# Kernel optimization log

Measured on AMD Instinct MI355X. Metric: run time of the kernel, lower is better.

Reference implementation:

```python
import jax, jax.numpy as jnp
import numpy as np

N, E, F_IN, H, C, L = 50000, 800000, 128, 128, 47, 3
BN_EPS = 1e-5


def setup_inputs() -> dict:
    key = jax.random.key(0)
    ks = jax.random.split(key, 12)
    s = 0.1
    return {
        "x": jax.random.normal(ks[0], (N, F_IN), jnp.float32),
        "edge_index": jax.random.randint(ks[1], (2, E), 0, N, jnp.int32),
        # stacked GINConv MLP params (in_channels == hidden so all layers stack)
        "W1": jax.random.normal(ks[2], (L, F_IN, H), jnp.float32) * s,
        "b1": jnp.full((L, H), 0.01, jnp.float32),
        "gamma": jnp.ones((L, H), jnp.float32),
        "beta": jnp.zeros((L, H), jnp.float32),
        "bn_mean": jnp.zeros((L, H), jnp.float32),
        "bn_var": jnp.ones((L, H), jnp.float32),
        "W2": jax.random.normal(ks[3], (L, H, H), jnp.float32) * s,
        "b2": jnp.full((L, H), 0.01, jnp.float32),
        # head
        "lw1": jax.random.normal(ks[4], (H, H), jnp.float32) * s,
        "lb1": jnp.zeros((H,), jnp.float32),
        "lw2": jax.random.normal(ks[5], (H, C), jnp.float32) * s,
        "lb2": jnp.zeros((C,), jnp.float32),
    }


def reference(x, edge_index, W1, b1, gamma, beta, bn_mean, bn_var, W2, b2, lw1, lb1, lw2, lb2):
    src, dst = edge_index[0], edge_index[1]
    h = x
    for i in range(L):
        # GINConv: nn((1 + eps) * x + sum_{j in N(i)} x_j), eps = 0
        agg = jax.ops.segment_sum(h[src], dst, num_segments=N)  # [N, H] scatter-sum
        z = agg + h
        z = z @ W1[i] + b1[i]
        # BatchNorm1d in eval mode (running stats)
        z = (z - bn_mean[i]) * jax.lax.rsqrt(bn_var[i] + BN_EPS) * gamma[i] + beta[i]
        z = jax.nn.relu(z)
        h = jax.nn.relu(z @ W2[i] + b2[i])
    h = jax.nn.relu(h @ lw1 + lb1)
    # dropout disabled (eval mode)
    logits = h @ lw2 + lb2
    return jax.nn.log_softmax(logits, axis=-1)
```

## Files before the change

### kernel.cpp

```cpp
#include <hip/hip_runtime.h>
#include <math.h>

#define NN 50000
#define EE 800000
#define HH 128
#define LL 3
#define CC 47
#define CAP 64
#define FILL_B 2048
#define NT_TILES 782

typedef _Float16 half8 __attribute__((ext_vector_type(8)));
typedef float    f32x4 __attribute__((ext_vector_type(4)));
typedef unsigned short us8 __attribute__((ext_vector_type(8)));

__device__ __forceinline__ f32x4 mfma16(half8 a, half8 b, f32x4 c) {
    return __builtin_amdgcn_mfma_f32_16x16x32_f16(a, b, c, 0, 0, 0);
}

__global__ void k_fill_prep(const int* __restrict__ ei, int* __restrict__ cursor,
                            unsigned short* __restrict__ csr,
                            const float* __restrict__ x, const float* __restrict__ W1,
                            const float* __restrict__ W2, const float* __restrict__ lw1,
                            const float* __restrict__ lw2, const float* __restrict__ b1,
                            const float* __restrict__ gamma, const float* __restrict__ beta,
                            const float* __restrict__ bnm, const float* __restrict__ bnv,
                            _Float16* __restrict__ xh, _Float16* __restrict__ hb0,
                            _Float16* __restrict__ hb1, _Float16* __restrict__ Wt1h,
                            _Float16* __restrict__ Wt2h, _Float16* __restrict__ lw1t,
                            _Float16* __restrict__ lw2t, float* __restrict__ A1f,
                            float* __restrict__ B1f) {
    if (blockIdx.x < FILL_B) {
        const int part = blockIdx.x & 7;
        const int chunk = blockIdx.x >> 3;
        const int nchunks = FILL_B >> 3;
        const int lo = part * (NN / 8);
        const int hi = (part == 7) ? NN : lo + (NN / 8);
        for (int e = chunk * 256 + threadIdx.x; e < EE; e += nchunks * 256) {
            const int d = ei[EE + e];
            if (d >= lo && d < hi) {
                const int pos = atomicAdd(&cursor[d], 1);
                if (pos < CAP) csr[(d << 6) + pos] = (unsigned short)ei[e];
            }
        }
        return;
    }
    const int i = (blockIdx.x - FILL_B) * 256 + threadIdx.x;
    const int Q0 = (NN * HH) / 8;
    const int Q1 = Q0 + LL * HH * HH;
    const int Q2 = Q1 + LL * HH * HH;
    const int Q3 = Q2 + HH * HH;
    const int Q4 = Q3 + 48 * HH;
    const int Q5 = Q4 + LL * HH;
    const int Q6 = Q5 + 3 * HH;
    if (i < Q0) {
        const f32x4* xp = (const f32x4*)x + (size_t)i * 2;
        f32x4 u = xp[0], v = xp[1];
        half8 o;
        o[0] = (_Float16)u[0]; o[1] = (_Float16)u[1]; o[2] = (_Float16)u[2]; o[3] = (_Float16)u[3];
        o[4] = (_Float16)v[0]; o[5] = (_Float16)v[1]; o[6] = (_Float16)v[2]; o[7] = (_Float16)v[3];
        *((half8*)xh + i) = o;
    } else if (i < Q1) {
        int j = i - Q0;
        int l = j / (HH * HH);
        int n = (j / HH) % HH;
        int k = j % HH;
        Wt1h[l * HH * HH + n * HH + k] = (_Float16)W1[l * HH * HH + k * HH + n];
    } else if (i < Q2) {
        int j = i - Q1;
        int l = j / (HH * HH);
        int n = (j / HH) % HH;
        int k = j % HH;
        Wt2h[l * HH * HH + n * HH + k] = (_Float16)W2[l * HH * HH + k * HH + n];
    } else if (i < Q3) {
        int j = i - Q2;
        int n = j / HH, k = j % HH;
        lw1t[n * HH + k] = (_Float16)lw1[k * HH + n];
    } else if (i < Q4) {
        int j = i - Q3;
        int n = j / HH, k = j % HH;
        lw2t[n * HH + k] = (_Float16)((n < CC) ? lw2[k * CC + n] : 0.f);
    } else if (i < Q5) {
        int j = i - Q4;
        float s = gamma[j] * rsqrtf(bnv[j] + 1e-5f);
        A1f[j] = s;
        B1f[j] = (b1[j] - bnm[j]) * s + beta[j];
    } else if (i < Q6) {
        int j = i - Q5;
        int b = j >> 7, k = j & 127;
        _Float16* t = (b == 0) ? xh : ((b == 1) ? hb0 : hb1);
        t[(size_t)NN * HH + k] = (_Float16)0.f;
    }
}

__device__ __forceinline__ void gather_tile(
    const _Float16* __restrict__ hin, const int* __restrict__ degs,
    const unsigned short* __restrict__ csr, _Float16* Ab, int tile0, int tid, int fo) {
#pragma unroll
    for (int pass = 0; pass < 4; ++pass) {
        const int r = pass * 16 + (tid >> 4);
        const int g = tile0 + r;
        const int gg = (g < NN) ? g : NN;
        float a[8];
        half8 hv = *(const half8*)(hin + (size_t)gg * HH + fo);
#pragma unroll
        for (int j = 0; j < 8; ++j) a[j] = (float)hv[j];
        int d = (g < NN) ? degs[g] : 0;
        d = (d < CAP) ? d : CAP;
        const unsigned short* crow = csr + (gg << 6);
        for (int kk = 0; kk < d; kk += 8) {
            us8 sv = *(const us8*)(crow + kk);
            int s[8];
#pragma unroll
            for (int j = 0; j < 8; ++j) s[j] = (kk + j < d) ? (int)sv[j] : NN;
            half8 v[8];
#pragma unroll
            for (int j = 0; j < 8; ++j) v[j] = *(const half8*)(hin + (size_t)s[j] * HH + fo);
#pragma unroll
            for (int j = 0; j < 8; ++j) {
#pragma unroll
                for (int t = 0; t < 8; ++t) a[t] += (float)v[j][t];
            }
        }
        half8 o;
#pragma unroll
        for (int j = 0; j < 8; ++j) o[j] = (_Float16)a[j];
        *(half8*)(Ab + r * 136 + fo) = o;
    }
}

__global__ __launch_bounds__(256, 4) void k_layer(
    const _Float16* __restrict__ hin, _Float16* __restrict__ hout,
    const _Float16* __restrict__ Wt1, const _Float16* __restrict__ Wt2,
    const float* __restrict__ A1, const float* __restrict__ B1,
    const float* __restrict__ b2, const int* __restrict__ degs,
    const unsigned short* __restrict__ csr) {
    __shared__ _Float16 Ab[64 * 136];
    const int tid = threadIdx.x;
    const int wave = tid >> 6, lane = tid & 63;
    const int q = lane >> 4, l15 = lane & 15;
    const int tile0 = blockIdx.x * 64;
    const int fo = (tid & 15) * 8;

    half8 Bf[2][4];
#pragma unroll
    for (int t = 0; t < 2; ++t)
#pragma unroll
        for (int kt = 0; kt < 4; ++kt)
            Bf[t][kt] = *(const half8*)(Wt1 + (wave * 32 + t * 16 + l15) * 128 + kt * 32 + q * 8);

    gather_tile(hin, degs, csr, Ab, tile0, tid, fo);
    __syncthreads();

    f32x4 acc[4][2];
#pragma unroll
    for (int s = 0; s < 4; ++s)
#pragma unroll
        for (int t = 0; t < 2; ++t) acc[s][t] = (f32x4){0.f, 0.f, 0.f, 0.f};
#pragma unroll
    for (int kt = 0; kt < 4; ++kt) {
        const int ko = kt * 32 + q * 8;
        half8 a0 = *(const half8*)(Ab + (0 * 16 + l15) * 136 + ko);
        half8 a1 = *(const half8*)(Ab + (1 * 16 + l15) * 136 + ko);
        half8 a2 = *(const half8*)(Ab + (2 * 16 + l15) * 136 + ko);
        half8 a3 = *(const half8*)(Ab + (3 * 16 + l15) * 136 + ko);
        acc[0][0] = mfma16(a0, Bf[0][kt], acc[0][0]);
        acc[1][0] = mfma16(a1, Bf[0][kt], acc[1][0]);
        acc[2][0] = mfma16(a2, Bf[0][kt], acc[2][0]);
        acc[3][0] = mfma16(a3, Bf[0][kt], acc[3][0]);
        acc[0][1] = mfma16(a0, Bf[1][kt], acc[0][1]);
        acc[1][1] = mfma16(a1, Bf[1][kt], acc[1][1]);
        acc[2][1] = mfma16(a2, Bf[1][kt], acc[2][1]);
        acc[3][1] = mfma16(a3, Bf[1][kt], acc[3][1]);
    }
#pragma unroll
    for (int t = 0; t < 2; ++t)
#pragma unroll
        for (int kt = 0; kt < 4; ++kt)
            Bf[t][kt] = *(const half8*)(Wt2 + (wave * 32 + t * 16 + l15) * 128 + kt * 32 + q * 8);
    __syncthreads();

#pragma unroll
    for (int t = 0; t < 2; ++t) {
        const int col = wave * 32 + t * 16 + l15;
        const float sc = A1[col], sh = B1[col];
#pragma unroll
        for (int s = 0; s < 4; ++s)
#pragma unroll
            for (int r = 0; r < 4; ++r) {
                const int row = s * 16 + q * 4 + r;
                float v = acc[s][t][r] * sc + sh;
                Ab[row * 136 + col] = (_Float16)fmaxf(v, 0.f);
            }
    }
    __syncthreads();

#pragma unroll
    for (int s = 0; s < 4; ++s)
#pragma unroll
        for (int t = 0; t < 2; ++t) acc[s][t] = (f32x4){0.f, 0.f, 0.f, 0.f};
#pragma unroll
    for (int kt = 0; kt < 4; ++kt) {
        const int ko = kt * 32 + q * 8;
        half8 a0 = *(const half8*)(Ab + (0 * 16 + l15) * 136 + ko);
        half8 a1 = *(const half8*)(Ab + (1 * 16 + l15) * 136 + ko);
        half8 a2 = *(const half8*)(Ab + (2 * 16 + l15) * 136 + ko);
        half8 a3 = *(const half8*)(Ab + (3 * 16 + l15) * 136 + ko);
        acc[0][0] = mfma16(a0, Bf[0][kt], acc[0][0]);
        acc[1][0] = mfma16(a1, Bf[0][kt], acc[1][0]);
        acc[2][0] = mfma16(a2, Bf[0][kt], acc[2][0]);
        acc[3][0] = mfma16(a3, Bf[0][kt], acc[3][0]);
        acc[0][1] = mfma16(a0, Bf[1][kt], acc[0][1]);
        acc[1][1] = mfma16(a1, Bf[1][kt], acc[1][1]);
        acc[2][1] = mfma16(a2, Bf[1][kt], acc[2][1]);
        acc[3][1] = mfma16(a3, Bf[1][kt], acc[3][1]);
    }
#pragma unroll
    for (int t = 0; t < 2; ++t) {
        const int col = wave * 32 + t * 16 + l15;
        const float bb = b2[col];
#pragma unroll
        for (int s = 0; s < 4; ++s)
#pragma unroll
            for (int r = 0; r < 4; ++r) {
                const int row = s * 16 + q * 4 + r;
                const int g = tile0 + row;
                if (g < NN) {
                    float v = fmaxf(acc[s][t][r] + bb, 0.f);
                    hout[(size_t)g * HH + col] = (_Float16)v;
                }
            }
    }
}

__global__ __launch_bounds__(256, 4) void k_layer_head(
    const _Float16* __restrict__ hin,
    const _Float16* __restrict__ Wt1, const _Float16* __restrict__ Wt2,
    const float* __restrict__ A1, const float* __restrict__ B1,
    const float* __restrict__ b2,
    const _Float16* __restrict__ lw1t, const _Float16* __restrict__ lw2t,
    const float* __restrict__ lb1, const float* __restrict__ lb2,
    float* __restrict__ out, const int* __restrict__ degs,
    const unsigned short* __restrict__ csr) {
    __shared__ _Float16 Ab[64 * 136];
    const int tid = threadIdx.x;
    const int wave = tid >> 6, lane = tid & 63;
    const int q = lane >> 4, l15 = lane & 15;
    const int tile0 = blockIdx.x * 64;
    const int fo = (tid & 15) * 8;

    half8 Bf[2][4];
#pragma unroll
    for (int t = 0; t < 2; ++t)
#pragma unroll
        for (int kt = 0; kt < 4; ++kt)
            Bf[t][kt] = *(const half8*)(Wt1 + (wave * 32 + t * 16 + l15) * 128 + kt * 32 + q * 8);

    gather_tile(hin, degs, csr, Ab, tile0, tid, fo);
    __syncthreads();

    f32x4 acc[4][2];
#pragma unroll
    for (int s = 0; s < 4; ++s)
#pragma unroll
        for (int t = 0; t < 2; ++t) acc[s][t] = (f32x4){0.f, 0.f, 0.f, 0.f};
#pragma unroll
    for (int kt = 0; kt < 4; ++kt) {
        const int ko = kt * 32 + q * 8;
        half8 a0 = *(const half8*)(Ab + (0 * 16 + l15) * 136 + ko);
        half8 a1 = *(const half8*)(Ab + (1 * 16 + l15) * 136 + ko);
        half8 a2 = *(const half8*)(Ab + (2 * 16 + l15) * 136 + ko);
        half8 a3 = *(const half8*)(Ab + (3 * 16 + l15) * 136 + ko);
        acc[0][0] = mfma16(a0, Bf[0][kt], acc[0][0]);
        acc[1][0] = mfma16(a1, Bf[0][kt], acc[1][0]);
        acc[2][0] = mfma16(a2, Bf[0][kt], acc[2][0]);
        acc[3][0] = mfma16(a3, Bf[0][kt], acc[3][0]);
        acc[0][1] = mfma16(a0, Bf[1][kt], acc[0][1]);
        acc[1][1] = mfma16(a1, Bf[1][kt], acc[1][1]);
        acc[2][1] = mfma16(a2, Bf[1][kt], acc[2][1]);
        acc[3][1] = mfma16(a3, Bf[1][kt], acc[3][1]);
    }
#pragma unroll
    for (int t = 0; t < 2; ++t)
#pragma unroll
        for (int kt = 0; kt < 4; ++kt)
            Bf[t][kt] = *(const half8*)(Wt2 + (wave * 32 + t * 16 + l15) * 128 + kt * 32 + q * 8);
    __syncthreads();
#pragma unroll
    for (int t = 0; t < 2; ++t) {
        const int col = wave * 32 + t * 16 + l15;
        const float sc = A1[col], sh = B1[col];
#pragma unroll
        for (int s = 0; s < 4; ++s)
#pragma unroll
            for (int r = 0; r < 4; ++r) {
                const int row = s * 16 + q * 4 + r;
                float v = acc[s][t][r] * sc + sh;
                Ab[row * 136 + col] = (_Float16)fmaxf(v, 0.f);
            }
    }
    __syncthreads();

#pragma unroll
    for (int s = 0; s < 4; ++s)
#pragma unroll
        for (int t = 0; t < 2; ++t) acc[s][t] = (f32x4){0.f, 0.f, 0.f, 0.f};
#pragma unroll
    for (int kt = 0; kt < 4; ++kt) {
        const int ko = kt * 32 + q * 8;
        half8 a0 = *(const half8*)(Ab + (0 * 16 + l15) * 136 + ko);
        half8 a1 = *(const half8*)(Ab + (1 * 16 + l15) * 136 + ko);
        half8 a2 = *(const half8*)(Ab + (2 * 16 + l15) * 136 + ko);
        half8 a3 = *(const half8*)(Ab + (3 * 16 + l15) * 136 + ko);
        acc[0][0] = mfma16(a0, Bf[0][kt], acc[0][0]);
        acc[1][0] = mfma16(a1, Bf[0][kt], acc[1][0]);
        acc[2][0] = mfma16(a2, Bf[0][kt], acc[2][0]);
        acc[3][0] = mfma16(a3, Bf[0][kt], acc[3][0]);
        acc[0][1] = mfma16(a0, Bf[1][kt], acc[0][1]);
        acc[1][1] = mfma16(a1, Bf[1][kt], acc[1][1]);
        acc[2][1] = mfma16(a2, Bf[1][kt], acc[2][1]);
        acc[3][1] = mfma16(a3, Bf[1][kt], acc[3][1]);
    }
#pragma unroll
    for (int t = 0; t < 2; ++t)
#pragma unroll
        for (int kt = 0; kt < 4; ++kt)
            Bf[t][kt] = *(const half8*)(lw1t + (wave * 32 + t * 16 + l15) * 128 + kt * 32 + q * 8);
    __syncthreads();
#pragma unroll
    for (int t = 0; t < 2; ++t) {
        const int col = wave * 32 + t * 16 + l15;
        const float bb = b2[col];
#pragma unroll
        for (int s = 0; s < 4; ++s)
#pragma unroll
            for (int r = 0; r < 4; ++r) {
                const int row = s * 16 + q * 4 + r;
                Ab[row * 136 + col] = (_Float16)fmaxf(acc[s][t][r] + bb, 0.f);
            }
    }
    __syncthreads();

#pragma unroll
    for (int s = 0; s < 4; ++s)
#pragma unroll
        for (int t = 0; t < 2; ++t) acc[s][t] = (f32x4){0.f, 0.f, 0.f, 0.f};
#pragma unroll
    for (int kt = 0; kt < 4; ++kt) {
        const int ko = kt * 32 + q * 8;
        half8 a0 = *(const half8*)(Ab + (0 * 16 + l15) * 136 + ko);
        half8 a1 = *(const half8*)(Ab + (1 * 16 + l15) * 136 + ko);
        half8 a2 = *(const half8*)(Ab + (2 * 16 + l15) * 136 + ko);
        half8 a3 = *(const half8*)(Ab + (3 * 16 + l15) * 136 + ko);
        acc[0][0] = mfma16(a0, Bf[0][kt], acc[0][0]);
        acc[1][0] = mfma16(a1, Bf[0][kt], acc[1][0]);
        acc[2][0] = mfma16(a2, Bf[0][kt], acc[2][0]);
        acc[3][0] = mfma16(a3, Bf[0][kt], acc[3][0]);
        acc[0][1] = mfma16(a0, Bf[1][kt], acc[0][1]);
        acc[1][1] = mfma16(a1, Bf[1][kt], acc[1][1]);
        acc[2][1] = mfma16(a2, Bf[1][kt], acc[2][1]);
        acc[3][1] = mfma16(a3, Bf[1][kt], acc[3][1]);
    }
    half8 Bh[4];
    if (wave < 3) {
#pragma unroll
        for (int kt = 0; kt < 4; ++kt)
            Bh[kt] = *(const half8*)(lw2t + (wave * 16 + l15) * 128 + kt * 32 + q * 8);
    }
    __syncthreads();
#pragma unroll
    for (int t = 0; t < 2; ++t) {
        const int col = wave * 32 + t * 16 + l15;
        const float bb = lb1[col];
#pragma unroll
        for (int s = 0; s < 4; ++s)
#pragma unroll
            for (int r = 0; r < 4; ++r) {
                const int row = s * 16 + q * 4 + r;
                Ab[row * 136 + col] = (_Float16)fmaxf(acc[s][t][r] + bb, 0.f);
            }
    }
    __syncthreads();

    f32x4 acc2[4];
#pragma unroll
    for (int s = 0; s < 4; ++s) acc2[s] = (f32x4){0.f, 0.f, 0.f, 0.f};
    if (wave < 3) {
#pragma unroll
        for (int kt = 0; kt < 4; ++kt) {
            const int ko = kt * 32 + q * 8;
            half8 a0 = *(const half8*)(Ab + (0 * 16 + l15) * 136 + ko);
            half8 a1 = *(const half8*)(Ab + (1 * 16 + l15) * 136 + ko);
            half8 a2 = *(const half8*)(Ab + (2 * 16 + l15) * 136 + ko);
            half8 a3 = *(const half8*)(Ab + (3 * 16 + l15) * 136 + ko);
            acc2[0] = mfma16(a0, Bh[kt], acc2[0]);
            acc2[1] = mfma16(a1, Bh[kt], acc2[1]);
            acc2[2] = mfma16(a2, Bh[kt], acc2[2]);
            acc2[3] = mfma16(a3, Bh[kt], acc2[3]);
        }
    }
    __syncthreads();

    float* Lb = (float*)Ab;
    if (wave < 3) {
        const int col = wave * 16 + l15;
        const float bb = (col < CC) ? lb2[col] : 0.f;
#pragma unroll
        for (int s = 0; s < 4; ++s)
#pragma unroll
            for (int r = 0; r < 4; ++r) {
                const int row = s * 16 + q * 4 + r;
                Lb[row * 49 + col] = acc2[s][r] + bb;
            }
    }
    __syncthreads();

    if (tid < 64) {
        const int g = tile0 + tid;
        if (g < NN) {
            float mx = -1e30f;
            for (int c = 0; c < CC; ++c) mx = fmaxf(mx, Lb[tid * 49 + c]);
            float ssum = 0.f;
            for (int c = 0; c < CC; ++c) ssum += expf(Lb[tid * 49 + c] - mx);
            const float ls = logf(ssum) + mx;
            for (int c = 0; c < CC; ++c) out[(size_t)g * CC + c] = Lb[tid * 49 + c] - ls;
        }
    }
}

extern "C" void kernel_launch(void* const* d_in, const int* in_sizes, int n_in,
                              void* d_out, int out_size, void* d_ws, size_t ws_size,
                              hipStream_t stream) {
    const float* x     = (const float*)d_in[0];
    const int*   ei    = (const int*)d_in[1];
    const float* W1    = (const float*)d_in[2];
    const float* b1    = (const float*)d_in[3];
    const float* gamma = (const float*)d_in[4];
    const float* beta  = (const float*)d_in[5];
    const float* bnm   = (const float*)d_in[6];
    const float* bnv   = (const float*)d_in[7];
    const float* W2    = (const float*)d_in[8];
    const float* b2    = (const float*)d_in[9];
    const float* lw1   = (const float*)d_in[10];
    const float* lb1   = (const float*)d_in[11];
    const float* lw2   = (const float*)d_in[12];
    const float* lb2   = (const float*)d_in[13];
    float* out = (float*)d_out;

    char* p = (char*)d_ws;
    auto carve = [&](size_t bytes) -> char* {
        char* r = p;
        p += (bytes + 255) & ~(size_t)255;
        return r;
    };
    int* cursor = (int*)carve((size_t)NN * 4);
    unsigned short* csr = (unsigned short*)carve((size_t)NN * CAP * 2);
    _Float16* Wt1h = (_Float16*)carve((size_t)LL * HH * HH * 2);
    _Float16* Wt2h = (_Float16*)carve((size_t)LL * HH * HH * 2);
    _Float16* lw1t = (_Float16*)carve((size_t)HH * HH * 2);
    _Float16* lw2t = (_Float16*)carve((size_t)48 * HH * 2);
    float* A1f = (float*)carve((size_t)LL * HH * 4);
    float* B1f = (float*)carve((size_t)LL * HH * 4);
    _Float16* xh  = (_Float16*)carve((size_t)(NN + 1) * HH * 2);
    _Float16* hb0 = (_Float16*)carve((size_t)(NN + 1) * HH * 2);
    _Float16* hb1 = (_Float16*)carve((size_t)(NN + 1) * HH * 2);

    hipMemsetAsync(cursor, 0, (size_t)NN * 4, stream);
    const int prep_total = (NN * HH) / 8 + 2 * LL * HH * HH + HH * HH + 48 * HH + LL * HH + 3 * HH;
    const int prep_blocks = (prep_total + 255) / 256;
    k_fill_prep<<<FILL_B + prep_blocks, 256, 0, stream>>>(
        ei, cursor, csr, x, W1, W2, lw1, lw2, b1, gamma, beta, bnm, bnv,
        xh, hb0, hb1, Wt1h, Wt2h, lw1t, lw2t, A1f, B1f);

    k_layer<<<NT_TILES, 256, 0, stream>>>(xh, hb0, Wt1h, Wt2h, A1f, B1f, b2,
                                          cursor, csr);
    k_layer<<<NT_TILES, 256, 0, stream>>>(hb0, hb1, Wt1h + HH * HH, Wt2h + HH * HH,
                                          A1f + HH, B1f + HH, b2 + HH,
                                          cursor, csr);
    k_layer_head<<<NT_TILES, 256, 0, stream>>>(hb1, Wt1h + 2 * HH * HH, Wt2h + 2 * HH * HH,
                                               A1f + 2 * HH, B1f + 2 * HH, b2 + 2 * HH,
                                               lw1t, lw2t, lb1, lb2, out,
                                               cursor, csr);
}
```

Baseline: 266.6 us.

## Store node features as FP8 to halve gather traffic

Node feature buffers (input x and the per-layer hidden states) are now kept in FP8 instead of FP16, and the neighbour gather decodes them with packed fp8-to-f32 conversions. Each layer's output tile is staged through shared memory so it can be packed and written to global memory as FP8. The aim is to halve the bytes moved by the bandwidth-bound neighbour gather and by the activation stores. The cost is a large loss of precision in the activations, which may exceed the accuracy tolerance, plus two extra barriers per tile.

```diff
diff --git a/kernel.cpp b/kernel.cpp
--- a/kernel.cpp
+++ b/kernel.cpp
@@ -12,10 +12,29 @@
 
 typedef _Float16 half8 __attribute__((ext_vector_type(8)));
 typedef float    f32x4 __attribute__((ext_vector_type(4)));
+typedef float    f32x2 __attribute__((ext_vector_type(2)));
+typedef unsigned int   u32x2 __attribute__((ext_vector_type(2)));
 typedef unsigned short us8 __attribute__((ext_vector_type(8)));
 
 __device__ __forceinline__ f32x4 mfma16(half8 a, half8 b, f32x4 c) {
     return __builtin_amdgcn_mfma_f32_16x16x32_f16(a, b, c, 0, 0, 0);
+}
+
+__device__ __forceinline__ void acc8_from_fp8(u32x2 w, float* a) {
+    f32x2 p0 = __builtin_amdgcn_cvt_pk_f32_fp8(w[0], false);
+    f32x2 p1 = __builtin_amdgcn_cvt_pk_f32_fp8(w[0], true);
+    f32x2 p2 = __builtin_amdgcn_cvt_pk_f32_fp8(w[1], false);
+    f32x2 p3 = __builtin_amdgcn_cvt_pk_f32_fp8(w[1], true);
+    a[0] += p0[0]; a[1] += p0[1]; a[2] += p1[0]; a[3] += p1[1];
+    a[4] += p2[0]; a[5] += p2[1]; a[6] += p3[0]; a[7] += p3[1];
+}
+__device__ __forceinline__ u32x2 pack8_fp8(const float* z) {
+    unsigned int lo = __builtin_amdgcn_cvt_pk_fp8_f32(z[0], z[1], 0, false);
+    lo = (unsigned int)__builtin_amdgcn_cvt_pk_fp8_f32(z[2], z[3], (int)lo, true);
+    unsigned int hi = __builtin_amdgcn_cvt_pk_fp8_f32(z[4], z[5], 0, false);
+    hi = (unsigned int)__builtin_amdgcn_cvt_pk_fp8_f32(z[6], z[7], (int)hi, true);
+    u32x2 w; w[0] = lo; w[1] = hi;
+    return w;
 }
 
 __global__ void k_fill_prep(const int* __restrict__ ei, int* __restrict__ cursor,
@@ -25,8 +44,8 @@
                             const float* __restrict__ lw2, const float* __restrict__ b1,
                             const float* __restrict__ gamma, const float* __restrict__ beta,
                             const float* __restrict__ bnm, const float* __restrict__ bnv,
-                            _Float16* __restrict__ xh, _Float16* __restrict__ hb0,
-                            _Float16* __restrict__ hb1, _Float16* __restrict__ Wt1h,
+                            unsigned char* __restrict__ x8, unsigned char* __restrict__ h8a,
+                            unsigned char* __restrict__ h8b, _Float16* __restrict__ Wt1h,
                             _Float16* __restrict__ Wt2h, _Float16* __restrict__ lw1t,
                             _Float16* __restrict__ lw2t, float* __restrict__ A1f,
                             float* __restrict__ B1f) {
@@ -56,10 +75,8 @@
     if (i < Q0) {
         const f32x4* xp = (const f32x4*)x + (size_t)i * 2;
         f32x4 u = xp[0], v = xp[1];
-        half8 o;
-        o[0] = (_Float16)u[0]; o[1] = (_Float16)u[1]; o[2] = (_Float16)u[2]; o[3] = (_Float16)u[3];
-        o[4] = (_Float16)v[0]; o[5] = (_Float16)v[1]; o[6] = (_Float16)v[2]; o[7] = (_Float16)v[3];
-        *((half8*)xh + i) = o;
+        float z[8] = {u[0], u[1], u[2], u[3], v[0], v[1], v[2], v[3]};
+        ((u32x2*)x8)[i] = pack8_fp8(z);
     } else if (i < Q1) {
         int j = i - Q0;
         int l = j / (HH * HH);
@@ -88,23 +105,22 @@
     } else if (i < Q6) {
         int j = i - Q5;
         int b = j >> 7, k = j & 127;
-        _Float16* t = (b == 0) ? xh : ((b == 1) ? hb0 : hb1);
-        t[(size_t)NN * HH + k] = (_Float16)0.f;
-    }
-}
-
-__device__ __forceinline__ void gather_tile(
-    const _Float16* __restrict__ hin, const int* __restrict__ degs,
+        unsigned char* t = (b == 0) ? x8 : ((b == 1) ? h8a : h8b);
+        t[(size_t)NN * HH + k] = 0;
+    }
+}
+
+__device__ __forceinline__ void gather_tile8(
+    const unsigned char* __restrict__ hin8, const int* __restrict__ degs,
     const unsigned short* __restrict__ csr, _Float16* Ab, int tile0, int tid, int fo) {
 #pragma unroll
     for (int pass = 0; pass < 4; ++pass) {
         const int r = pass * 16 + (tid >> 4);
         const int g = tile0 + r;
         const int gg = (g < NN) ? g : NN;
-        float a[8];
-        half8 hv = *(const half8*)(hin + (size_t)gg * HH + fo);
-#pragma unroll
-        for (int j = 0; j < 8; ++j) a[j] = (float)hv[j];
+        float a[8] = {0.f, 0.f, 0.f, 0.f, 0.f, 0.f, 0.f, 0.f};
+        u32x2 hv = *(const u32x2*)(hin8 + (size_t)gg * HH + fo);
+        acc8_from_fp8(hv, a);
         int d = (g < NN) ? degs[g] : 0;
         d = (d < CAP) ? d : CAP;
         const unsigned short* crow = csr + (gg << 6);
@@ -113,14 +129,11 @@
             int s[8];
 #pragma unroll
             for (int j = 0; j < 8; ++j) s[j] = (kk + j < d) ? (int)sv[j] : NN;
-            half8 v[8];
-#pragma unroll
-            for (int j = 0; j < 8; ++j) v[j] = *(const half8*)(hin + (size_t)s[j] * HH + fo);
-#pragma unroll
-            for (int j = 0; j < 8; ++j) {
-#pragma unroll
-                for (int t = 0; t < 8; ++t) a[t] += (float)v[j][t];
-            }
+            u32x2 v[8];
+#pragma unroll
+            for (int j = 0; j < 8; ++j) v[j] = *(const u32x2*)(hin8 + (size_t)s[j] * HH + fo);
+#pragma unroll
+            for (int j = 0; j < 8; ++j) acc8_from_fp8(v[j], a);
         }
         half8 o;
 #pragma unroll
@@ -130,7 +143,7 @@
 }
 
 __global__ __launch_bounds__(256, 4) void k_layer(
-    const _Float16* __restrict__ hin, _Float16* __restrict__ hout,
+    const unsigned char* __restrict__ hin8, unsigned char* __restrict__ hout8,
     const _Float16* __restrict__ Wt1, const _Float16* __restrict__ Wt2,
     const float* __restrict__ A1, const float* __restrict__ B1,
     const float* __restrict__ b2, const int* __restrict__ degs,
@@ -149,7 +162,7 @@
         for (int kt = 0; kt < 4; ++kt)
             Bf[t][kt] = *(const half8*)(Wt1 + (wave * 32 + t * 16 + l15) * 128 + kt * 32 + q * 8);
 
-    gather_tile(hin, degs, csr, Ab, tile0, tid, fo);
+    gather_tile8(hin8, degs, csr, Ab, tile0, tid, fo);
     __syncthreads();
 
     f32x4 acc[4][2];
@@ -215,6 +228,8 @@
         acc[2][1] = mfma16(a2, Bf[1][kt], acc[2][1]);
         acc[3][1] = mfma16(a3, Bf[1][kt], acc[3][1]);
     }
+    __syncthreads();
+
 #pragma unroll
     for (int t = 0; t < 2; ++t) {
         const int col = wave * 32 + t * 16 + l15;
@@ -224,17 +239,27 @@
 #pragma unroll
             for (int r = 0; r < 4; ++r) {
                 const int row = s * 16 + q * 4 + r;
-                const int g = tile0 + row;
-                if (g < NN) {
-                    float v = fmaxf(acc[s][t][r] + bb, 0.f);
-                    hout[(size_t)g * HH + col] = (_Float16)v;
-                }
-            }
+                Ab[row * 136 + col] = (_Float16)fmaxf(acc[s][t][r] + bb, 0.f);
+            }
+    }
+    __syncthreads();
+
+#pragma unroll
+    for (int pass = 0; pass < 4; ++pass) {
+        const int r = pass * 16 + (tid >> 4);
+        const int g = tile0 + r;
+        if (g < NN) {
+            half8 z = *(const half8*)(Ab + r * 136 + fo);
+            float zf[8];
+#pragma unroll
+            for (int j = 0; j < 8; ++j) zf[j] = (float)z[j];
+            *(u32x2*)(hout8 + (size_t)g * HH + fo) = pack8_fp8(zf);
+        }
     }
 }
 
 __global__ __launch_bounds__(256, 4) void k_layer_head(
-    const _Float16* __restrict__ hin,
+    const unsigned char* __restrict__ hin8,
     const _Float16* __restrict__ Wt1, const _Float16* __restrict__ Wt2,
     const float* __restrict__ A1, const float* __restrict__ B1,
     const float* __restrict__ b2,
@@ -256,7 +281,7 @@
         for (int kt = 0; kt < 4; ++kt)
             Bf[t][kt] = *(const half8*)(Wt1 + (wave * 32 + t * 16 + l15) * 128 + kt * 32 + q * 8);
 
-    gather_tile(hin, degs, csr, Ab, tile0, tid, fo);
+    gather_tile8(hin8, degs, csr, Ab, tile0, tid, fo);
     __syncthreads();
 
     f32x4 acc[4][2];
@@ -461,23 +486,23 @@
     _Float16* lw2t = (_Float16*)carve((size_t)48 * HH * 2);
     float* A1f = (float*)carve((size_t)LL * HH * 4);
     float* B1f = (float*)carve((size_t)LL * HH * 4);
-    _Float16* xh  = (_Float16*)carve((size_t)(NN + 1) * HH * 2);
-    _Float16* hb0 = (_Float16*)carve((size_t)(NN + 1) * HH * 2);
-    _Float16* hb1 = (_Float16*)carve((size_t)(NN + 1) * HH * 2);
+    unsigned char* x8  = (unsigned char*)carve((size_t)(NN + 1) * HH);
+    unsigned char* h8a = (unsigned char*)carve((size_t)(NN + 1) * HH);
+    unsigned char* h8b = (unsigned char*)carve((size_t)(NN + 1) * HH);
 
     hipMemsetAsync(cursor, 0, (size_t)NN * 4, stream);
     const int prep_total = (NN * HH) / 8 + 2 * LL * HH * HH + HH * HH + 48 * HH + LL * HH + 3 * HH;
     const int prep_blocks = (prep_total + 255) / 256;
     k_fill_prep<<<FILL_B + prep_blocks, 256, 0, stream>>>(
         ei, cursor, csr, x, W1, W2, lw1, lw2, b1, gamma, beta, bnm, bnv,
-        xh, hb0, hb1, Wt1h, Wt2h, lw1t, lw2t, A1f, B1f);
-
-    k_layer<<<NT_TILES, 256, 0, stream>>>(xh, hb0, Wt1h, Wt2h, A1f, B1f, b2,
+        x8, h8a, h8b, Wt1h, Wt2h, lw1t, lw2t, A1f, B1f);
+
+    k_layer<<<NT_TILES, 256, 0, stream>>>(x8, h8a, Wt1h, Wt2h, A1f, B1f, b2,
                                           cursor, csr);
-    k_layer<<<NT_TILES, 256, 0, stream>>>(hb0, hb1, Wt1h + HH * HH, Wt2h + HH * HH,
+    k_layer<<<NT_TILES, 256, 0, stream>>>(h8a, h8b, Wt1h + HH * HH, Wt2h + HH * HH,
                                           A1f + HH, B1f + HH, b2 + HH,
                                           cursor, csr);
-    k_layer_head<<<NT_TILES, 256, 0, stream>>>(hb1, Wt1h + 2 * HH * HH, Wt2h + 2 * HH * HH,
+    k_layer_head<<<NT_TILES, 256, 0, stream>>>(h8b, Wt1h + 2 * HH * HH, Wt2h + 2 * HH * HH,
                                                A1f + 2 * HH, B1f + 2 * HH, b2 + 2 * HH,
                                                lw1t, lw2t, lb1, lb2, out,
                                                cursor, csr);
```

Result: faster. 231.3 us (-13.2%).
